# Kernel tuning notes

Measured on AMD Instinct MI355X. Metric: run time of the kernel, lower is better.

The kernel has to match this reference:

```python
import jax, jax.numpy as jnp
import numpy as np

G, H, D = 8, 16, 64           # groups, heads-per-group, head_size
B, S = 2, 1024                # sequences, tokens per sequence (T = B*S packed)
HID = G * H * D               # 8192
SCALE = D ** -0.5


def _rotary(x, cos, sin):
    # NeoX-style rotary. x: [T, nh, D]; cos/sin: [T, D//2]
    half = D // 2
    c = cos[:, None, :]
    s = sin[:, None, :]
    x1, x2 = x[..., :half], x[..., half:]
    return jnp.concatenate([x1 * c - x2 * s, x2 * c + x1 * s], axis=-1)


def setup_inputs() -> dict:
    key = jax.random.key(0)
    ks = jax.random.split(key, 6)
    T = B * S
    hidden_states = jax.random.normal(ks[0], (T, HID), jnp.float32)
    # true rotary tables from positions (base 10000)
    pos = jnp.tile(jnp.arange(S, dtype=jnp.float32), B)            # [T]
    inv_freq = 1.0 / (10000.0 ** (jnp.arange(0, D, 2, dtype=jnp.float32) / D))
    freqs = pos[:, None] * inv_freq[None, :]                       # [T, D//2]
    cos, sin = jnp.cos(freqs), jnp.sin(freqs)
    w_qkv = jax.random.normal(ks[1], (HID, G * (H + 2) * D), jnp.float32) * (HID ** -0.5)
    b_qkv = jax.random.normal(ks[2], (G * (H + 2) * D,), jnp.float32) * 0.02
    w_dense = jax.random.normal(ks[3], (G * H * D, HID), jnp.float32) * (HID ** -0.5)
    b_dense = jax.random.normal(ks[4], (HID,), jnp.float32) * 0.02
    kv_cache = jnp.zeros((2, 4096, G, D), jnp.float32)
    slots = jnp.arange(T, dtype=jnp.int32)
    return dict(hidden_states=hidden_states, cos=cos, sin=sin,
                w_qkv=w_qkv, b_qkv=b_qkv, w_dense=w_dense, b_dense=b_dense,
                kv_cache=kv_cache, slots=slots, batch_size=B)


def reference(hidden_states, cos, sin, w_qkv, b_qkv, w_dense, b_dense,
              kv_cache, slots, batch_size):
    T = hidden_states.shape[0]
    qkv = hidden_states @ w_qkv + b_qkv                    # [T, G*(H+2)*D]
    qkv = qkv.reshape(T, G, H + 2, D)
    query = qkv[:, :, :H, :].reshape(T, G * H, D)          # [T, G*H, D]
    k = qkv[:, :, H, :]                                    # [T, G, D]
    v = qkv[:, :, H + 1, :]                                # [T, G, D]

    query = _rotary(query, cos, sin)
    k = _rotary(k, cos, sin)

    # reshape_and_cache: write rotated K and V into the slot cache
    new_cache = kv_cache.at[0, slots].set(k).at[1, slots].set(v)

    # prefill flash attention, causal, GQA (each group's K/V shared by H heads)
    q = query.reshape(batch_size, S, G, H, D)
    kb = k.reshape(batch_size, S, G, D)
    vb = v.reshape(batch_size, S, G, D)
    scores = jnp.einsum('bsghd,btgd->bghst', q, kb) * SCALE  # [B,G,H,S,S]
    causal = jnp.tril(jnp.ones((S, S), bool))
    scores = jnp.where(causal, scores, jnp.finfo(scores.dtype).min)
    probs = jax.nn.softmax(scores, axis=-1)
    attn = jnp.einsum('bghst,btgd->bsghd', probs, vb)        # [B,S,G,H,D]
    attn = attn.reshape(T, G * H * D)
    out = attn @ w_dense + b_dense                           # [T, HID]
    return out, new_cache
```

## Files before the change

kernel.cpp:

```cpp
#include <hip/hip_runtime.h>

#define T_TOK 2048
#define HIDD  8192
#define NQKV  9216
#define GG    8
#define HH    16
#define DD    64
#define SS    1024
#define BB    2
#define SCALE_ATTN 0.125f

typedef __attribute__((ext_vector_type(4))) float f32x4;
typedef __attribute__((ext_vector_type(8))) short bf16x8;

#define GLOBAL_AS __attribute__((address_space(1)))
#define LDS_AS    __attribute__((address_space(3)))

__device__ __forceinline__ void glds16(const void* g, void* l) {
  __builtin_amdgcn_global_load_lds((GLOBAL_AS void*)(g), (LDS_AS void*)(l), 16, 0, 0);
}

__device__ __forceinline__ ushort f2bf(float f) {
  union { float f; unsigned u; } v; v.f = f;
  unsigned u = v.u + 0x7fffu + ((v.u >> 16) & 1u);
  return (ushort)(u >> 16);
}

__global__ void cvt_bf16_kernel(const float* __restrict__ in, ushort* __restrict__ out, int n4) {
  int i = blockIdx.x * 256 + threadIdx.x;
  if (i >= n4) return;
  float4 v = ((const float4*)in)[i];
  ushort4 o;
  o.x = f2bf(v.x); o.y = f2bf(v.y); o.z = f2bf(v.z); o.w = f2bf(v.w);
  ((ushort4*)out)[i] = o;
}

__global__ void copy_f32_kernel(const float* __restrict__ in, float* __restrict__ out, int n4) {
  int i = blockIdx.x * 256 + threadIdx.x;
  if (i < n4) ((float4*)out)[i] = ((const float4*)in)[i];
}

__global__ void transpose_bf16_kernel(const float* __restrict__ in, ushort* __restrict__ out,
                                      int R, int C) {
  __shared__ float tile[32][33];
  const int c0 = blockIdx.x * 32, r0 = blockIdx.y * 32;
  const int tx = threadIdx.x, ty = threadIdx.y;
  #pragma unroll
  for (int i = ty; i < 32; i += 8)
    tile[i][tx] = in[(size_t)(r0 + i) * C + (c0 + tx)];
  __syncthreads();
  #pragma unroll
  for (int i = ty; i < 32; i += 8)
    out[(size_t)(c0 + i) * R + (r0 + tx)] = f2bf(tile[tx][i]);
}

__global__ __launch_bounds__(256, 2) void gemm_bt_kernel(
    const ushort* __restrict__ A, const ushort* __restrict__ Bt,
    const float* __restrict__ bias, float* __restrict__ C,
    int M, int N, int K)
{
  __shared__ __align__(16) ushort As[128 * 32];
  __shared__ __align__(16) ushort Bs[128 * 32];
  const int tid = threadIdx.x;
  const int wid = tid >> 6, lane = tid & 63;
  const int kg = lane >> 4, ln = lane & 15;
  const int m0 = blockIdx.y * 128, n0 = blockIdx.x * 128;
  const int wm = (wid >> 1) * 64, wn = (wid & 1) * 64;

  f32x4 acc[4][4] = {};

  const int e_base = wid * 1024;
  const int e0 = e_base + lane * 8;
  const int e1 = e_base + 512 + lane * 8;
  const int r0a = e0 >> 5, c0a = e0 & 31;
  const int r1a = e1 >> 5, c1a = e1 & 31;

  const ushort* Ap0 = A + (size_t)(m0 + r0a) * K + c0a;
  const ushort* Ap1 = A + (size_t)(m0 + r1a) * K + c1a;
  const ushort* Bp0 = Bt + (size_t)(n0 + r0a) * K + c0a;
  const ushort* Bp1 = Bt + (size_t)(n0 + r1a) * K + c1a;
  ushort* lA0 = &As[e_base];
  ushort* lA1 = &As[e_base + 512];
  ushort* lB0 = &Bs[e_base];
  ushort* lB1 = &Bs[e_base + 512];

  for (int k0 = 0; k0 < K; k0 += 32) {
    glds16(Ap0 + k0, lA0);
    glds16(Ap1 + k0, lA1);
    glds16(Bp0 + k0, lB0);
    glds16(Bp1 + k0, lB1);
    __syncthreads();
    bf16x8 af[4], bfr[4];
    #pragma unroll
    for (int t = 0; t < 4; ++t) {
      af[t]  = *(const bf16x8*)&As[(wm + t * 16 + ln) * 32 + kg * 8];
      bfr[t] = *(const bf16x8*)&Bs[(wn + t * 16 + ln) * 32 + kg * 8];
    }
    #pragma unroll
    for (int i = 0; i < 4; ++i)
      #pragma unroll
      for (int j = 0; j < 4; ++j)
        acc[i][j] = __builtin_amdgcn_mfma_f32_16x16x32_bf16(af[i], bfr[j], acc[i][j], 0, 0, 0);
    __syncthreads();
  }

  #pragma unroll
  for (int i = 0; i < 4; ++i) {
    const int row = m0 + wm + i * 16 + kg * 4;
    #pragma unroll
    for (int j = 0; j < 4; ++j) {
      const int col = n0 + wn + j * 16 + ln;
      const float bv = bias[col];
      #pragma unroll
      for (int r = 0; r < 4; ++r)
        C[(size_t)(row + r) * N + col] = acc[i][j][r] + bv;
    }
  }
}

__global__ void rotary_scatter_kernel(const float* __restrict__ qkv,
                                      const float* __restrict__ cosb, const float* __restrict__ sinb,
                                      const int* __restrict__ slots,
                                      ushort* __restrict__ Qr, ushort* __restrict__ Kr,
                                      ushort* __restrict__ Vr, float* __restrict__ cache)
{
  const int t = blockIdx.x;
  const int slot = slots[t];
  for (int j = threadIdx.x; j < GG * 18 * 32; j += 256) {
    const int g = j / 576;
    const int rem = j - g * 576;
    const int head = rem >> 5;
    const int d = rem & 31;
    const float* row = qkv + (size_t)t * NQKV + g * 1152 + head * 64;
    const float x1 = row[d], x2 = row[d + 32];
    const float c = cosb[t * 32 + d], s = sinb[t * 32 + d];
    if (head < 16) {
      const size_t o = ((size_t)t * 128 + g * 16 + head) * 64;
      Qr[o + d]      = f2bf(x1 * c - x2 * s);
      Qr[o + 32 + d] = f2bf(x2 * c + x1 * s);
    } else if (head == 16) {
      const float o1 = x1 * c - x2 * s, o2 = x2 * c + x1 * s;
      const size_t o = ((size_t)t * GG + g) * 64;
      Kr[o + d] = f2bf(o1); Kr[o + 32 + d] = f2bf(o2);
      const size_t co = ((size_t)slot * GG + g) * 64;
      cache[co + d] = o1; cache[co + 32 + d] = o2;
    } else {
      const size_t o = ((size_t)t * GG + g) * 64;
      Vr[o + d] = f2bf(x1); Vr[o + 32 + d] = f2bf(x2);
      const size_t co = (size_t)4096 * GG * 64 + ((size_t)slot * GG + g) * 64;
      cache[co + d] = x1; cache[co + 32 + d] = x2;
    }
  }
}

__global__ __launch_bounds__(256, 2) void flash_attn_kernel(
    const ushort* __restrict__ Q, const ushort* __restrict__ Kc,
    const ushort* __restrict__ Vc, ushort* __restrict__ O)
{
  const int qb = blockIdx.x;
  const int gh = blockIdx.y;
  const int g  = gh >> 4;
  const int b  = blockIdx.z;
  const int tid = threadIdx.x;
  const int wid = tid >> 6, lane = tid & 63;
  const int kg = lane >> 4, ln = lane & 15;

  __shared__ __align__(16) ushort Ks[64 * 72];
  __shared__ __align__(16) ushort Vt[64 * 72];
  __shared__ __align__(16) ushort Ps[64 * 72];

  const int sq = qb * 64 + wid * 16 + ln;
  const size_t qoff = ((size_t)(b * SS + sq) * 128 + gh) * 64;
  const bf16x8 qf0 = *(const bf16x8*)&Q[qoff + kg * 8];
  const bf16x8 qf1 = *(const bf16x8*)&Q[qoff + 32 + kg * 8];

  f32x4 acc_o[4] = {};
  float m_i[4], l_i[4];
  #pragma unroll
  for (int r = 0; r < 4; ++r) { m_i[r] = -1e30f; l_i[r] = 0.f; }

  const int srow = qb * 64 + wid * 16 + kg * 4;

  for (int it = 0; it <= qb; ++it) {
    const int t0 = it * 64;
    __syncthreads();
    #pragma unroll
    for (int rep = 0; rep < 2; ++rep) {
      const int u = rep * 256 + tid;
      const int tt = u >> 3;
      const int d0 = (u & 7) * 8;
      const size_t src = ((size_t)(b * SS + t0 + tt) * GG + g) * 64 + d0;
      *(uint4*)&Ks[tt * 72 + d0] = *(const uint4*)&Kc[src];
      bf16x8 vv = *(const bf16x8*)&Vc[src];
      #pragma unroll
      for (int jj = 0; jj < 8; ++jj)
        Vt[(d0 + jj) * 72 + tt] = ((const ushort*)&vv)[jj];
    }
    __syncthreads();

    f32x4 sc[4];
    #pragma unroll
    for (int tt = 0; tt < 4; ++tt) {
      bf16x8 kf0 = *(const bf16x8*)&Ks[(tt * 16 + ln) * 72 + kg * 8];
      bf16x8 kf1 = *(const bf16x8*)&Ks[(tt * 16 + ln) * 72 + 32 + kg * 8];
      f32x4 z = {};
      z = __builtin_amdgcn_mfma_f32_16x16x32_bf16(qf0, kf0, z, 0, 0, 0);
      z = __builtin_amdgcn_mfma_f32_16x16x32_bf16(qf1, kf1, z, 0, 0, 0);
      sc[tt] = z;
    }

    if (it == qb) {
      #pragma unroll
      for (int tt = 0; tt < 4; ++tt) {
        const int tg = t0 + tt * 16 + ln;
        #pragma unroll
        for (int r = 0; r < 4; ++r)
          sc[tt][r] = (tg <= srow + r) ? sc[tt][r] * SCALE_ATTN : -1e30f;
      }
    } else {
      #pragma unroll
      for (int tt = 0; tt < 4; ++tt)
        #pragma unroll
        for (int r = 0; r < 4; ++r)
          sc[tt][r] *= SCALE_ATTN;
    }

    float alpha[4];
    #pragma unroll
    for (int r = 0; r < 4; ++r) {
      float mx = fmaxf(fmaxf(sc[0][r], sc[1][r]), fmaxf(sc[2][r], sc[3][r]));
      #pragma unroll
      for (int off = 1; off < 16; off <<= 1)
        mx = fmaxf(mx, __shfl_xor(mx, off, 64));
      const float mn = fmaxf(m_i[r], mx);
      float rs = 0.f;
      #pragma unroll
      for (int tt = 0; tt < 4; ++tt) {
        const float p = __expf(sc[tt][r] - mn);
        sc[tt][r] = p; rs += p;
      }
      #pragma unroll
      for (int off = 1; off < 16; off <<= 1)
        rs += __shfl_xor(rs, off, 64);
      alpha[r] = __expf(m_i[r] - mn);
      l_i[r] = l_i[r] * alpha[r] + rs;
      m_i[r] = mn;
    }
    #pragma unroll
    for (int dt = 0; dt < 4; ++dt)
      #pragma unroll
      for (int r = 0; r < 4; ++r)
        acc_o[dt][r] *= alpha[r];

    #pragma unroll
    for (int tt = 0; tt < 4; ++tt)
      #pragma unroll
      for (int r = 0; r < 4; ++r)
        Ps[(wid * 16 + kg * 4 + r) * 72 + tt * 16 + ln] = f2bf(sc[tt][r]);
    __syncthreads();

    #pragma unroll
    for (int c = 0; c < 2; ++c) {
      bf16x8 pf = *(const bf16x8*)&Ps[(wid * 16 + ln) * 72 + c * 32 + kg * 8];
      #pragma unroll
      for (int dt = 0; dt < 4; ++dt) {
        bf16x8 vf = *(const bf16x8*)&Vt[(dt * 16 + ln) * 72 + c * 32 + kg * 8];
        acc_o[dt] = __builtin_amdgcn_mfma_f32_16x16x32_bf16(pf, vf, acc_o[dt], 0, 0, 0);
      }
    }
  }

  #pragma unroll
  for (int dt = 0; dt < 4; ++dt) {
    #pragma unroll
    for (int r = 0; r < 4; ++r) {
      const float o = acc_o[dt][r] / l_i[r];
      O[((size_t)(b * SS + srow + r) * 128 + gh) * 64 + dt * 16 + ln] = f2bf(o);
    }
  }
}

#define WS0_HB   ((size_t)0)
#define WS1_WT   ((size_t)33554432)
#define WS2_QKV  ((size_t)(33554432 + 150994944))
#define WS3_QR   (WS2_QKV + (size_t)75497472)
#define WS4_KR   (WS3_QR + (size_t)33554432)
#define WS5_VR   (WS4_KR + (size_t)2097152)

extern "C" void kernel_launch(void* const* d_in, const int* in_sizes, int n_in,
                              void* d_out, int out_size, void* d_ws, size_t ws_size,
                              hipStream_t stream) {
  const float* hidden  = (const float*)d_in[0];
  const float* cosb    = (const float*)d_in[1];
  const float* sinb    = (const float*)d_in[2];
  const float* w_qkv   = (const float*)d_in[3];
  const float* b_qkv   = (const float*)d_in[4];
  const float* w_dense = (const float*)d_in[5];
  const float* b_dense = (const float*)d_in[6];
  const float* kv_in   = (const float*)d_in[7];
  const int*   slots   = (const int*)d_in[8];

  float* out = (float*)d_out;
  float* out_cache = out + (size_t)T_TOK * HIDD;

  char* ws = (char*)d_ws;
  ushort* hb   = (ushort*)(ws + WS0_HB);
  ushort* wT   = (ushort*)(ws + WS1_WT);
  float*  qkv  = (float*)(ws + WS2_QKV);
  ushort* qr   = (ushort*)(ws + WS3_QR);
  ushort* kr   = (ushort*)(ws + WS4_KR);
  ushort* vr   = (ushort*)(ws + WS5_VR);
  ushort* attn = hb;

  cvt_bf16_kernel<<<(T_TOK * HIDD / 4 + 255) / 256, 256, 0, stream>>>(hidden, hb, T_TOK * HIDD / 4);
  transpose_bf16_kernel<<<dim3(NQKV / 32, HIDD / 32), dim3(32, 8), 0, stream>>>(w_qkv, wT, HIDD, NQKV);
  gemm_bt_kernel<<<dim3(NQKV / 128, T_TOK / 128), 256, 0, stream>>>(hb, wT, b_qkv, qkv, T_TOK, NQKV, HIDD);
  copy_f32_kernel<<<(2 * 4096 * GG * DD / 4 + 255) / 256, 256, 0, stream>>>(kv_in, out_cache, 2 * 4096 * GG * DD / 4);
  rotary_scatter_kernel<<<T_TOK, 256, 0, stream>>>(qkv, cosb, sinb, slots, qr, kr, vr, out_cache);
  transpose_bf16_kernel<<<dim3(HIDD / 32, HIDD / 32), dim3(32, 8), 0, stream>>>(w_dense, wT, HIDD, HIDD);
  flash_attn_kernel<<<dim3(SS / 64, GG * HH, BB), 256, 0, stream>>>(qr, kr, vr, attn);
  gemm_bt_kernel<<<dim3(HIDD / 128, T_TOK / 128), 256, 0, stream>>>(attn, wT, b_dense, out, T_TOK, HIDD, HIDD);
}
```

Measured before the change: 1.839 ms.

## Vectorize weight transpose, relayout Q/K/V, and double query tile per attention block

The weight transpose now uses 64x64 tiles with float4 loads and ushort4 stores instead of scalar 32x32 accesses. The rotary kernel writes Q and K head-major per sequence and writes V pre-transposed (d-major), so attention can load K and V tiles with plain 16-byte copies and no scalar transpose into shared memory. The attention kernel now covers 128 query rows per block, two 16-row subtiles per wave, so each K/V tile is reused twice, and launch bounds move from 2 to 4 blocks. The costs are higher register pressure and fewer blocks with coarser causal load balance, and the V write in the rotary kernel becomes strided.

Result: faster. 1.788 ms (-2.8%).

```diff
diff --git a/kernel.cpp b/kernel.cpp
--- a/kernel.cpp
+++ b/kernel.cpp
@@ -40,18 +40,32 @@
   if (i < n4) ((float4*)out)[i] = ((const float4*)in)[i];
 }
 
-__global__ void transpose_bf16_kernel(const float* __restrict__ in, ushort* __restrict__ out,
-                                      int R, int C) {
-  __shared__ float tile[32][33];
-  const int c0 = blockIdx.x * 32, r0 = blockIdx.y * 32;
-  const int tx = threadIdx.x, ty = threadIdx.y;
-  #pragma unroll
-  for (int i = ty; i < 32; i += 8)
-    tile[i][tx] = in[(size_t)(r0 + i) * C + (c0 + tx)];
+__global__ __launch_bounds__(256) void transpose_bf16_kernel(
+    const float* __restrict__ in, ushort* __restrict__ out, int R, int C)
+{
+  __shared__ float tile[64][65];
+  const int c0 = blockIdx.x * 64, r0 = blockIdx.y * 64;
+  const int tid = threadIdx.x;
+  const int tx = tid & 15, iy = tid >> 4;
+  #pragma unroll
+  for (int p = 0; p < 4; ++p) {
+    const int i = iy + p * 16;
+    const float4 v = *(const float4*)&in[(size_t)(r0 + i) * C + c0 + tx * 4];
+    tile[i][tx * 4 + 0] = v.x; tile[i][tx * 4 + 1] = v.y;
+    tile[i][tx * 4 + 2] = v.z; tile[i][tx * 4 + 3] = v.w;
+  }
   __syncthreads();
-  #pragma unroll
-  for (int i = ty; i < 32; i += 8)
-    out[(size_t)(c0 + i) * R + (r0 + tx)] = f2bf(tile[tx][i]);
+  const int r4 = tid & 15, cg = tid >> 4;
+  #pragma unroll
+  for (int p = 0; p < 4; ++p) {
+    const int c = cg + p * 16;
+    ushort4 o;
+    o.x = f2bf(tile[r4 * 4 + 0][c]);
+    o.y = f2bf(tile[r4 * 4 + 1][c]);
+    o.z = f2bf(tile[r4 * 4 + 2][c]);
+    o.w = f2bf(tile[r4 * 4 + 3][c]);
+    *(ushort4*)&out[(size_t)(c0 + c) * R + r0 + r4 * 4] = o;
+  }
 }
 
 __global__ __launch_bounds__(256, 2) void gemm_bt_kernel(
@@ -125,6 +139,7 @@
                                       ushort* __restrict__ Vr, float* __restrict__ cache)
 {
   const int t = blockIdx.x;
+  const int b = t >> 10, s = t & 1023;
   const int slot = slots[t];
   for (int j = threadIdx.x; j < GG * 18 * 32; j += 256) {
     const int g = j / 576;
@@ -133,27 +148,28 @@
     const int d = rem & 31;
     const float* row = qkv + (size_t)t * NQKV + g * 1152 + head * 64;
     const float x1 = row[d], x2 = row[d + 32];
-    const float c = cosb[t * 32 + d], s = sinb[t * 32 + d];
+    const float c = cosb[t * 32 + d], s_ = sinb[t * 32 + d];
     if (head < 16) {
-      const size_t o = ((size_t)t * 128 + g * 16 + head) * 64;
-      Qr[o + d]      = f2bf(x1 * c - x2 * s);
-      Qr[o + 32 + d] = f2bf(x2 * c + x1 * s);
+      const size_t o = ((size_t)((b * 128 + g * 16 + head) * 1024 + s)) * 64;
+      Qr[o + d]      = f2bf(x1 * c - x2 * s_);
+      Qr[o + 32 + d] = f2bf(x2 * c + x1 * s_);
     } else if (head == 16) {
-      const float o1 = x1 * c - x2 * s, o2 = x2 * c + x1 * s;
-      const size_t o = ((size_t)t * GG + g) * 64;
+      const float o1 = x1 * c - x2 * s_, o2 = x2 * c + x1 * s_;
+      const size_t o = ((size_t)((b * 8 + g) * 1024 + s)) * 64;
       Kr[o + d] = f2bf(o1); Kr[o + 32 + d] = f2bf(o2);
       const size_t co = ((size_t)slot * GG + g) * 64;
       cache[co + d] = o1; cache[co + 32 + d] = o2;
     } else {
-      const size_t o = ((size_t)t * GG + g) * 64;
-      Vr[o + d] = f2bf(x1); Vr[o + 32 + d] = f2bf(x2);
+      const size_t vo = ((size_t)((b * 8 + g) * 64 + d)) * 1024 + s;
+      Vr[vo] = f2bf(x1);
+      Vr[vo + (size_t)32 * 1024] = f2bf(x2);
       const size_t co = (size_t)4096 * GG * 64 + ((size_t)slot * GG + g) * 64;
       cache[co + d] = x1; cache[co + 32 + d] = x2;
     }
   }
 }
 
-__global__ __launch_bounds__(256, 2) void flash_attn_kernel(
+__global__ __launch_bounds__(256, 4) void flash_attn_kernel(
     const ushort* __restrict__ Q, const ushort* __restrict__ Kc,
     const ushort* __restrict__ Vc, ushort* __restrict__ O)
 {
@@ -167,115 +183,138 @@
 
   __shared__ __align__(16) ushort Ks[64 * 72];
   __shared__ __align__(16) ushort Vt[64 * 72];
-  __shared__ __align__(16) ushort Ps[64 * 72];
-
-  const int sq = qb * 64 + wid * 16 + ln;
-  const size_t qoff = ((size_t)(b * SS + sq) * 128 + gh) * 64;
-  const bf16x8 qf0 = *(const bf16x8*)&Q[qoff + kg * 8];
-  const bf16x8 qf1 = *(const bf16x8*)&Q[qoff + 32 + kg * 8];
-
-  f32x4 acc_o[4] = {};
-  float m_i[4], l_i[4];
-  #pragma unroll
-  for (int r = 0; r < 4; ++r) { m_i[r] = -1e30f; l_i[r] = 0.f; }
-
-  const int srow = qb * 64 + wid * 16 + kg * 4;
-
-  for (int it = 0; it <= qb; ++it) {
+  __shared__ __align__(16) ushort Ps[128 * 72];
+
+  bf16x8 qf[2][2];
+  #pragma unroll
+  for (int st = 0; st < 2; ++st) {
+    const int sq = qb * 128 + wid * 32 + st * 16 + ln;
+    const size_t qoff = ((size_t)((b * 128 + gh) * 1024 + sq)) * 64;
+    qf[st][0] = *(const bf16x8*)&Q[qoff + kg * 8];
+    qf[st][1] = *(const bf16x8*)&Q[qoff + 32 + kg * 8];
+  }
+
+  f32x4 acc_o[2][4] = {};
+  float m_i[2][4], l_i[2][4];
+  #pragma unroll
+  for (int st = 0; st < 2; ++st)
+    #pragma unroll
+    for (int r = 0; r < 4; ++r) { m_i[st][r] = -1e30f; l_i[st][r] = 0.f; }
+
+  const size_t kbase = ((size_t)(b * 8 + g) * 1024) * 64;
+  const size_t vbase = ((size_t)(b * 8 + g) * 64) * 1024;
+
+  const int n_it = 2 * qb + 2;
+  for (int it = 0; it < n_it; ++it) {
     const int t0 = it * 64;
     __syncthreads();
     #pragma unroll
     for (int rep = 0; rep < 2; ++rep) {
-      const int u = rep * 256 + tid;
-      const int tt = u >> 3;
-      const int d0 = (u & 7) * 8;
-      const size_t src = ((size_t)(b * SS + t0 + tt) * GG + g) * 64 + d0;
-      *(uint4*)&Ks[tt * 72 + d0] = *(const uint4*)&Kc[src];
-      bf16x8 vv = *(const bf16x8*)&Vc[src];
-      #pragma unroll
-      for (int jj = 0; jj < 8; ++jj)
-        Vt[(d0 + jj) * 72 + tt] = ((const ushort*)&vv)[jj];
-    }
-    __syncthreads();
-
-    f32x4 sc[4];
+      const int idx = rep * 256 + tid;
+      const int rr = idx >> 3, c8 = (idx & 7) * 8;
+      *(uint4*)&Ks[rr * 72 + c8] = *(const uint4*)&Kc[kbase + (size_t)(t0 + rr) * 64 + c8];
+      *(uint4*)&Vt[rr * 72 + c8] = *(const uint4*)&Vc[vbase + (size_t)rr * 1024 + t0 + c8];
+    }
+    __syncthreads();
+
+    f32x4 sc[2][4];
     #pragma unroll
     for (int tt = 0; tt < 4; ++tt) {
-      bf16x8 kf0 = *(const bf16x8*)&Ks[(tt * 16 + ln) * 72 + kg * 8];
-      bf16x8 kf1 = *(const bf16x8*)&Ks[(tt * 16 + ln) * 72 + 32 + kg * 8];
-      f32x4 z = {};
-      z = __builtin_amdgcn_mfma_f32_16x16x32_bf16(qf0, kf0, z, 0, 0, 0);
-      z = __builtin_amdgcn_mfma_f32_16x16x32_bf16(qf1, kf1, z, 0, 0, 0);
-      sc[tt] = z;
-    }
-
-    if (it == qb) {
-      #pragma unroll
-      for (int tt = 0; tt < 4; ++tt) {
-        const int tg = t0 + tt * 16 + ln;
+      const bf16x8 kf0 = *(const bf16x8*)&Ks[(tt * 16 + ln) * 72 + kg * 8];
+      const bf16x8 kf1 = *(const bf16x8*)&Ks[(tt * 16 + ln) * 72 + 32 + kg * 8];
+      #pragma unroll
+      for (int st = 0; st < 2; ++st) {
+        f32x4 z = {};
+        z = __builtin_amdgcn_mfma_f32_16x16x32_bf16(qf[st][0], kf0, z, 0, 0, 0);
+        z = __builtin_amdgcn_mfma_f32_16x16x32_bf16(qf[st][1], kf1, z, 0, 0, 0);
+        sc[st][tt] = z;
+      }
+    }
+
+    if (it >= 2 * qb) {
+      #pragma unroll
+      for (int st = 0; st < 2; ++st) {
+        const int srow = qb * 128 + wid * 32 + st * 16 + kg * 4;
+        #pragma unroll
+        for (int tt = 0; tt < 4; ++tt) {
+          const int tg = t0 + tt * 16 + ln;
+          #pragma unroll
+          for (int r = 0; r < 4; ++r)
+            sc[st][tt][r] = (tg <= srow + r) ? sc[st][tt][r] * SCALE_ATTN : -1e30f;
+        }
+      }
+    } else {
+      #pragma unroll
+      for (int st = 0; st < 2; ++st)
+        #pragma unroll
+        for (int tt = 0; tt < 4; ++tt)
+          #pragma unroll
+          for (int r = 0; r < 4; ++r)
+            sc[st][tt][r] *= SCALE_ATTN;
+    }
+
+    #pragma unroll
+    for (int st = 0; st < 2; ++st) {
+      float alpha[4];
+      #pragma unroll
+      for (int r = 0; r < 4; ++r) {
+        float mx = fmaxf(fmaxf(sc[st][0][r], sc[st][1][r]), fmaxf(sc[st][2][r], sc[st][3][r]));
+        #pragma unroll
+        for (int off = 1; off < 16; off <<= 1)
+          mx = fmaxf(mx, __shfl_xor(mx, off, 64));
+        const float mn = fmaxf(m_i[st][r], mx);
+        float rs = 0.f;
+        #pragma unroll
+        for (int tt = 0; tt < 4; ++tt) {
+          const float p = __expf(sc[st][tt][r] - mn);
+          sc[st][tt][r] = p; rs += p;
+        }
+        #pragma unroll
+        for (int off = 1; off < 16; off <<= 1)
+          rs += __shfl_xor(rs, off, 64);
+        alpha[r] = __expf(m_i[st][r] - mn);
+        l_i[st][r] = l_i[st][r] * alpha[r] + rs;
+        m_i[st][r] = mn;
+      }
+      #pragma unroll
+      for (int dt = 0; dt < 4; ++dt)
         #pragma unroll
         for (int r = 0; r < 4; ++r)
-          sc[tt][r] = (tg <= srow + r) ? sc[tt][r] * SCALE_ATTN : -1e30f;
-      }
-    } else {
+          acc_o[st][dt][r] *= alpha[r];
       #pragma unroll
       for (int tt = 0; tt < 4; ++tt)
         #pragma unroll
         for (int r = 0; r < 4; ++r)
-          sc[tt][r] *= SCALE_ATTN;
-    }
-
-    float alpha[4];
-    #pragma unroll
-    for (int r = 0; r < 4; ++r) {
-      float mx = fmaxf(fmaxf(sc[0][r], sc[1][r]), fmaxf(sc[2][r], sc[3][r]));
-      #pragma unroll
-      for (int off = 1; off < 16; off <<= 1)
-        mx = fmaxf(mx, __shfl_xor(mx, off, 64));
-      const float mn = fmaxf(m_i[r], mx);
-      float rs = 0.f;
-      #pragma unroll
-      for (int tt = 0; tt < 4; ++tt) {
-        const float p = __expf(sc[tt][r] - mn);
-        sc[tt][r] = p; rs += p;
-      }
-      #pragma unroll
-      for (int off = 1; off < 16; off <<= 1)
-        rs += __shfl_xor(rs, off, 64);
-      alpha[r] = __expf(m_i[r] - mn);
-      l_i[r] = l_i[r] * alpha[r] + rs;
-      m_i[r] = mn;
-    }
-    #pragma unroll
-    for (int dt = 0; dt < 4; ++dt)
-      #pragma unroll
-      for (int r = 0; r < 4; ++r)
-        acc_o[dt][r] *= alpha[r];
-
-    #pragma unroll
-    for (int tt = 0; tt < 4; ++tt)
-      #pragma unroll
-      for (int r = 0; r < 4; ++r)
-        Ps[(wid * 16 + kg * 4 + r) * 72 + tt * 16 + ln] = f2bf(sc[tt][r]);
+          Ps[(wid * 32 + st * 16 + kg * 4 + r) * 72 + tt * 16 + ln] = f2bf(sc[st][tt][r]);
+    }
     __syncthreads();
 
     #pragma unroll
     for (int c = 0; c < 2; ++c) {
-      bf16x8 pf = *(const bf16x8*)&Ps[(wid * 16 + ln) * 72 + c * 32 + kg * 8];
-      #pragma unroll
-      for (int dt = 0; dt < 4; ++dt) {
-        bf16x8 vf = *(const bf16x8*)&Vt[(dt * 16 + ln) * 72 + c * 32 + kg * 8];
-        acc_o[dt] = __builtin_amdgcn_mfma_f32_16x16x32_bf16(pf, vf, acc_o[dt], 0, 0, 0);
-      }
-    }
-  }
-
-  #pragma unroll
-  for (int dt = 0; dt < 4; ++dt) {
-    #pragma unroll
-    for (int r = 0; r < 4; ++r) {
-      const float o = acc_o[dt][r] / l_i[r];
-      O[((size_t)(b * SS + srow + r) * 128 + gh) * 64 + dt * 16 + ln] = f2bf(o);
+      bf16x8 vf[4];
+      #pragma unroll
+      for (int dt = 0; dt < 4; ++dt)
+        vf[dt] = *(const bf16x8*)&Vt[(dt * 16 + ln) * 72 + c * 32 + kg * 8];
+      #pragma unroll
+      for (int st = 0; st < 2; ++st) {
+        const bf16x8 pf = *(const bf16x8*)&Ps[(wid * 32 + st * 16 + ln) * 72 + c * 32 + kg * 8];
+        #pragma unroll
+        for (int dt = 0; dt < 4; ++dt)
+          acc_o[st][dt] = __builtin_amdgcn_mfma_f32_16x16x32_bf16(pf, vf[dt], acc_o[st][dt], 0, 0, 0);
+      }
+    }
+  }
+
+  #pragma unroll
+  for (int st = 0; st < 2; ++st) {
+    const int srow = qb * 128 + wid * 32 + st * 16 + kg * 4;
+    #pragma unroll
+    for (int dt = 0; dt < 4; ++dt) {
+      #pragma unroll
+      for (int r = 0; r < 4; ++r) {
+        const float o = acc_o[st][dt][r] / l_i[st][r];
+        O[((size_t)(b * 1024 + srow + r)) * 8192 + gh * 64 + dt * 16 + ln] = f2bf(o);
+      }
     }
   }
 }
@@ -313,11 +352,11 @@
   ushort* attn = hb;
 
   cvt_bf16_kernel<<<(T_TOK * HIDD / 4 + 255) / 256, 256, 0, stream>>>(hidden, hb, T_TOK * HIDD / 4);
-  transpose_bf16_kernel<<<dim3(NQKV / 32, HIDD / 32), dim3(32, 8), 0, stream>>>(w_qkv, wT, HIDD, NQKV);
+  transpose_bf16_kernel<<<dim3(NQKV / 64, HIDD / 64), 256, 0, stream>>>(w_qkv, wT, HIDD, NQKV);
   gemm_bt_kernel<<<dim3(NQKV / 128, T_TOK / 128), 256, 0, stream>>>(hb, wT, b_qkv, qkv, T_TOK, NQKV, HIDD);
   copy_f32_kernel<<<(2 * 4096 * GG * DD / 4 + 255) / 256, 256, 0, stream>>>(kv_in, out_cache, 2 * 4096 * GG * DD / 4);
   rotary_scatter_kernel<<<T_TOK, 256, 0, stream>>>(qkv, cosb, sinb, slots, qr, kr, vr, out_cache);
-  transpose_bf16_kernel<<<dim3(HIDD / 32, HIDD / 32), dim3(32, 8), 0, stream>>>(w_dense, wT, HIDD, HIDD);
-  flash_attn_kernel<<<dim3(SS / 64, GG * HH, BB), 256, 0, stream>>>(qr, kr, vr, attn);
+  transpose_bf16_kernel<<<dim3(HIDD / 64, HIDD / 64), 256, 0, stream>>>(w_dense, wT, HIDD, HIDD);
+  flash_attn_kernel<<<dim3(SS / 128, GG * HH, BB), 256, 0, stream>>>(qr, kr, vr, attn);
   gemm_bt_kernel<<<dim3(HIDD / 128, T_TOK / 128), 256, 0, stream>>>(attn, wT, b_dense, out, T_TOK, HIDD, HIDD);
 }
```
